# Optimization experiments

Measured on AMD Instinct MI355X. Metric: run time of the kernel, lower is better.

## Reference

```python
import jax, jax.numpy as jnp
import numpy as np

N = 50000          # nodes
E = 1_600_000      # edges
IN_DIM = 64
HID = 64
HEADS = 2
EDGE_DIM = 8
OUT_DIM = 2
NEG_SLOPE = 0.2    # PyG GATConv default negative_slope


def _gat_params(key, in_ch, out_ch, heads, edge_dim, concat):
    ks = jax.random.split(key, 6)
    s = 0.1
    W = jax.random.normal(ks[0], (in_ch, heads * out_ch), jnp.float32) * s
    a_src = jax.random.normal(ks[1], (heads, out_ch), jnp.float32) * s
    a_dst = jax.random.normal(ks[2], (heads, out_ch), jnp.float32) * s
    We = jax.random.normal(ks[3], (edge_dim, heads * out_ch), jnp.float32) * s
    a_e = jax.random.normal(ks[4], (heads, out_ch), jnp.float32) * s
    b = jnp.zeros((heads * out_ch if concat else out_ch,), jnp.float32)
    return W, a_src, a_dst, We, a_e, b


def gat_conv(x, edge_index, edge_attr, W, a_src, a_dst, We, a_e, b, heads, out_ch, concat):
    # Faithful PyG GATConv with edge_dim, add_self_loops=True, fill_value='mean'.
    n = x.shape[0]
    src0, dst0 = edge_index[0], edge_index[1]
    # self-loop edge_attr = mean of incoming edge attrs (scatter-mean over dst)
    cnt = jax.ops.segment_sum(jnp.ones((src0.shape[0],), x.dtype), dst0, num_segments=n)
    loop_attr = jax.ops.segment_sum(edge_attr, dst0, num_segments=n) / jnp.maximum(cnt, 1.0)[:, None]
    loop = jnp.arange(n, dtype=src0.dtype)
    src = jnp.concatenate([src0, loop])
    dst = jnp.concatenate([dst0, loop])
    ea = jnp.concatenate([edge_attr, loop_attr], axis=0)          # [E+N, edge_dim]

    h = (x @ W).reshape(n, heads, out_ch)                          # [N, H, C]
    al_src = jnp.einsum('nhc,hc->nh', h, a_src)                    # [N, H]
    al_dst = jnp.einsum('nhc,hc->nh', h, a_dst)
    e = (ea @ We).reshape(-1, heads, out_ch)                       # [E+N, H, C]
    al_edge = jnp.einsum('ehc,hc->eh', e, a_e)

    alpha = jax.nn.leaky_relu(al_src[src] + al_dst[dst] + al_edge, NEG_SLOPE)  # [E+N, H]
    # segment softmax over destination node (every dst has a self loop)
    amax = jax.ops.segment_max(alpha, dst, num_segments=n)
    ex = jnp.exp(alpha - amax[dst])
    denom = jax.ops.segment_sum(ex, dst, num_segments=n)
    w = ex / (denom[dst] + 1e-16)

    out = jax.ops.segment_sum(h[src] * w[:, :, None], dst, num_segments=n)     # [N, H, C]
    out = out.reshape(n, heads * out_ch) if concat else out.mean(axis=1)
    return out + b


def setup_inputs() -> dict:
    key = jax.random.key(0)
    ks = jax.random.split(key, 8)
    inp = {
        'x': jax.random.normal(ks[0], (N, IN_DIM), jnp.float32),
        'edge_index': jax.random.randint(ks[1], (2, E), 0, N, dtype=jnp.int32),
        'edge_attr': jax.random.normal(ks[2], (E, EDGE_DIM), jnp.float32),
    }
    # layer 0: in -> hid, heads=1, concat=True
    for name, p in zip(['W0', 'as0', 'ad0', 'We0', 'ae0', 'b0'], _gat_params(ks[3], IN_DIM, HID, 1, EDGE_DIM, True)):
        inp[name] = p
    # layers 1,2: hid -> hid, heads=HEADS, concat=False
    for name, p in zip(['W1', 'as1', 'ad1', 'We1', 'ae1', 'b1'], _gat_params(ks[4], HID, HID, HEADS, EDGE_DIM, False)):
        inp[name] = p
    for name, p in zip(['W2', 'as2', 'ad2', 'We2', 'ae2', 'b2'], _gat_params(ks[5], HID, HID, HEADS, EDGE_DIM, False)):
        inp[name] = p
    # final: hid -> out_dim, heads=1, concat=True
    for name, p in zip(['W3', 'as3', 'ad3', 'We3', 'ae3', 'b3'], _gat_params(ks[6], HID, OUT_DIM, 1, EDGE_DIM, True)):
        inp[name] = p
    return inp


def reference(x, edge_index, edge_attr,
              W0, as0, ad0, We0, ae0, b0,
              W1, as1, ad1, We1, ae1, b1,
              W2, as2, ad2, We2, ae2, b2,
              W3, as3, ad3, We3, ae3, b3):
    h = jax.nn.relu(gat_conv(x, edge_index, edge_attr, W0, as0, ad0, We0, ae0, b0, 1, HID, True))
    h = jax.nn.relu(gat_conv(h, edge_index, edge_attr, W1, as1, ad1, We1, ae1, b1, HEADS, HID, False))
    h = jax.nn.relu(gat_conv(h, edge_index, edge_attr, W2, as2, ad2, We2, ae2, b2, HEADS, HID, False))
    return gat_conv(h, edge_index, edge_attr, W3, as3, ad3, We3, ae3, b3, 1, OUT_DIM, True)
```

## Files before the change

### kernel.cpp

```cpp
#include <hip/hip_runtime.h>
#include <math.h>


#define GSZ 256
#define CAPB 10240
#define CHUNK 4096
#define CAP_C 9984

__device__ __forceinline__ float wave_sum64(float v) {
#pragma unroll
  for (int o = 32; o >= 1; o >>= 1) v += __shfl_xor(v, o);
  return v;
}
__device__ __forceinline__ float dot8(const float4& a, const float4& b,
                                      const float* c) {
  return a.x * c[0] + a.y * c[1] + a.z * c[2] + a.w * c[3] + b.x * c[4] +
         b.y * c[5] + b.z * c[6] + b.w * c[7];
}


__global__ __launch_bounds__(256) void bin_kernel(const int* __restrict__ src,
                                                  const int* __restrict__ dst,
                                                  int* __restrict__ bfill,
                                                  int2* __restrict__ bbuf,
                                                  int E_) {
  __shared__ int histo[256];
  __shared__ int scanb[256];
  __shared__ int segstart[256];
  __shared__ int gbase[256];
  __shared__ int cur[256];
  __shared__ int2 stage[CHUNK];
  __shared__ int gtarg[CHUNK];
  const int t = threadIdx.x;
  const int e0 = blockIdx.x * CHUNK;
  const int cnt = min(CHUNK, E_ - e0);
  histo[t] = 0;
  __syncthreads();
  int myd[CHUNK / 256];
#pragma unroll
  for (int k = 0; k < CHUNK / 256; ++k) {
    int i = t + k * 256;
    int d = -1;
    if (i < cnt) {
      d = dst[e0 + i];
      atomicAdd(&histo[d >> 8], 1);
    }
    myd[k] = d;
  }
  __syncthreads();
  const int v = histo[t];
  int acc = v;
  scanb[t] = v;
  __syncthreads();
#pragma unroll
  for (int o = 1; o < 256; o <<= 1) {
    int u = (t >= o) ? scanb[t - o] : 0;
    __syncthreads();
    acc += u;
    scanb[t] = acc;
    __syncthreads();
  }
  int gp = 0;
  if (v > 0) gp = atomicAdd(&bfill[t], v);
  segstart[t] = acc - v;
  gbase[t] = t * CAPB + min(gp, CAPB - v);
  cur[t] = 0;
  __syncthreads();
#pragma unroll
  for (int k = 0; k < CHUNK / 256; ++k) {
    int i = t + k * 256;
    int d = myd[k];
    if (d >= 0) {
      int b = d >> 8;
      int s = src[e0 + i];
      int p = atomicAdd(&cur[b], 1);
      int sl = segstart[b] + p;
      stage[sl] = make_int2(s, (e0 + i) | ((d & 255) << 21));
      gtarg[sl] = gbase[b] + p;
    }
  }
  __syncthreads();
  for (int i = t; i < cnt; i += 256) bbuf[gtarg[i]] = stage[i];
}

__global__ __launch_bounds__(256) void count_kernel(
    const int* __restrict__ bfill, const int2* __restrict__ bbuf,
    int* __restrict__ cnt, int n) {
  __shared__ int h[256];
  const int b = blockIdx.x;
  const int t = threadIdx.x;
  h[t] = 0;
  __syncthreads();
  const int m = min(bfill[b], CAPB);
  const int2* reg = bbuf + (size_t)b * CAPB;
  for (int i = t; i < m; i += 256) {
    int dl = ((unsigned)reg[i].y) >> 21;
    atomicAdd(&h[dl], 1);
  }
  __syncthreads();
  int node = b * GSZ + t;
  if (node < n) cnt[node] = h[t];
}

__global__ __launch_bounds__(256) void scan1_kernel(const int* __restrict__ cnt,
                                                    int* __restrict__ rowp,
                                                    int* __restrict__ bsum,
                                                    int n) {
  __shared__ int sd[256];
  const int t = threadIdx.x;
  const int base = blockIdx.x * 1024 + t * 4;
  int v0 = (base + 0 < n) ? cnt[base + 0] + 1 : 0;
  int v1 = (base + 1 < n) ? cnt[base + 1] + 1 : 0;
  int v2 = (base + 2 < n) ? cnt[base + 2] + 1 : 0;
  int v3 = (base + 3 < n) ? cnt[base + 3] + 1 : 0;
  const int s = v0 + v1 + v2 + v3;
  sd[t] = s;
  __syncthreads();
  int acc = s;
#pragma unroll
  for (int o = 1; o < 256; o <<= 1) {
    int u = (t >= o) ? sd[t - o] : 0;
    __syncthreads();
    acc += u;
    sd[t] = acc;
    __syncthreads();
  }
  int excl = acc - s;
  if (base + 0 < n) rowp[base + 0] = excl;
  if (base + 1 < n) rowp[base + 1] = excl + v0;
  if (base + 2 < n) rowp[base + 2] = excl + v0 + v1;
  if (base + 3 < n) rowp[base + 3] = excl + v0 + v1 + v2;
  if (t == 255) bsum[blockIdx.x] = acc;
}

__global__ void scan2_kernel(int* __restrict__ bsum, int nb) {
  const int lane = threadIdx.x;
  int v = (lane < nb) ? bsum[lane] : 0;
  int incl = v;
#pragma unroll
  for (int o = 1; o < 64; o <<= 1) {
    int u = __shfl_up(incl, o);
    if (lane >= o) incl += u;
  }
  if (lane < nb) bsum[lane] = incl - v;
  if (lane == 63) bsum[nb] = incl;
}

__global__ void scan3_kernel(int* __restrict__ rowp,
                             const int* __restrict__ bsum, int n, int nb) {
  int i = blockIdx.x * 256 + threadIdx.x;
  if (i >= n) return;
  rowp[i] += bsum[i >> 10];
  if (i == 0) rowp[n] = bsum[nb];
}

__global__ __launch_bounds__(256) void place_kernel(
    const int* __restrict__ rowp, const int* __restrict__ bfill,
    const int2* __restrict__ bbuf, int* __restrict__ col_src,
    int* __restrict__ eidA, int n, int E_) {
  __shared__ int rp[GSZ + 1];
  __shared__ int cur[GSZ];
  __shared__ int2 stage[CAP_C];
  const int b = blockIdx.x;
  const int t = threadIdx.x;
  const int lo = b * GSZ;
  const int nk = min(GSZ, n - lo);
  for (int i = t; i <= nk; i += 256) rp[i] = rowp[lo + i];
  cur[t] = 0;
  __syncthreads();
  const int s0 = rp[0];
  const int span = rp[nk] - s0;
  const bool fits = (span <= CAP_C);
  const int m = min(bfill[b], CAPB);
  const int2* reg = bbuf + (size_t)b * CAPB;
  for (int i = t; i < m; i += 256) {
    int2 pl = reg[i];
    int dl = ((unsigned)pl.y) >> 21;
    int e2 = pl.y & 0x1FFFFF;
    int p = atomicAdd(&cur[dl], 1);
    int slot = rp[dl] + p;
    if (fits) stage[slot - s0] = make_int2(pl.x, e2);
    else { col_src[slot] = pl.x; eidA[slot] = e2; }
  }
  if (t < nk) {
    int slot = rp[t + 1] - 1;
    int node = lo + t;
    if (fits) stage[slot - s0] = make_int2(node, E_ + node);
    else { col_src[slot] = node; eidA[slot] = E_ + node; }
  }
  __syncthreads();
  if (fits) {
    for (int i = t; i < span; i += 256) {
      int2 v = stage[i];
      col_src[s0 + i] = v.x;
      eidA[s0 + i] = v.y;
    }
  }
}

__global__ void comb_all_kernel(const float* __restrict__ We0,
                                const float* __restrict__ ae0,
                                const float* __restrict__ We1,
                                const float* __restrict__ ae1,
                                const float* __restrict__ We2,
                                const float* __restrict__ ae2,
                                const float* __restrict__ We3,
                                const float* __restrict__ ae3,
                                float* __restrict__ comb) {
  int t = threadIdx.x;
  if (t >= 48) return;
  float s = 0.f;
  if (t < 8) {
    int d = t;
    for (int c = 0; c < 64; ++c) s += We0[d * 64 + c] * ae0[c];
  } else if (t < 24) {
    int idx = t - 8, h = idx >> 3, d = idx & 7;
    for (int c = 0; c < 64; ++c) s += We1[d * 128 + h * 64 + c] * ae1[h * 64 + c];
  } else if (t < 40) {
    int idx = t - 24, h = idx >> 3, d = idx & 7;
    for (int c = 0; c < 64; ++c) s += We2[d * 128 + h * 64 + c] * ae2[h * 64 + c];
  } else {
    int d = t - 40;
    for (int c = 0; c < 2; ++c) s += We3[d * 2 + c] * ae3[c];
  }
  comb[t] = s;
}

__global__ __launch_bounds__(256) void edge_prep_kernel(
    const int* __restrict__ row_ptr, const int* __restrict__ eid,
    const float* __restrict__ ea, const float* __restrict__ comb,
    float* __restrict__ edot0, float* __restrict__ edot1,
    float* __restrict__ edot2, float* __restrict__ edot3, int n, int E_) {
  __shared__ float cb[48];
  if (threadIdx.x < 48) cb[threadIdx.x] = comb[threadIdx.x];
  __syncthreads();
  const int lane = threadIdx.x & 63;
  const int node = blockIdx.x * 4 + (threadIdx.x >> 6);
  if (node >= n) return;

  const int start = row_ptr[node];
  const int selfpos = row_ptr[node + 1] - 1;

  float s0 = 0.f, s1 = 0.f, s2 = 0.f, s3 = 0.f, s4 = 0.f, s5 = 0.f, s6 = 0.f,
        s7 = 0.f;
  for (int i = start + lane; i < selfpos; i += 64) {
    int id = eid[i];
    const float4* v = reinterpret_cast<const float4*>(ea + (size_t)id * 8);
    float4 a = v[0], b = v[1];
    s0 += a.x; s1 += a.y; s2 += a.z; s3 += a.w;
    s4 += b.x; s5 += b.y; s6 += b.z; s7 += b.w;
    edot0[i] = dot8(a, b, cb + 0);
    edot1[2 * i + 0] = dot8(a, b, cb + 8);
    edot1[2 * i + 1] = dot8(a, b, cb + 16);
    edot2[2 * i + 0] = dot8(a, b, cb + 24);
    edot2[2 * i + 1] = dot8(a, b, cb + 32);
    edot3[i] = dot8(a, b, cb + 40);
  }
#pragma unroll
  for (int o = 32; o >= 1; o >>= 1) {
    s0 += __shfl_xor(s0, o); s1 += __shfl_xor(s1, o);
    s2 += __shfl_xor(s2, o); s3 += __shfl_xor(s3, o);
    s4 += __shfl_xor(s4, o); s5 += __shfl_xor(s5, o);
    s6 += __shfl_xor(s6, o); s7 += __shfl_xor(s7, o);
  }
  if (lane == 0) {
    float deg = (float)(selfpos - start);
    float inv = 1.f / fmaxf(deg, 1.f);
    float4 a = make_float4(s0 * inv, s1 * inv, s2 * inv, s3 * inv);
    float4 b = make_float4(s4 * inv, s5 * inv, s6 * inv, s7 * inv);
    int i = selfpos;
    edot0[i] = dot8(a, b, cb + 0);
    edot1[2 * i + 0] = dot8(a, b, cb + 8);
    edot1[2 * i + 1] = dot8(a, b, cb + 16);
    edot2[2 * i + 0] = dot8(a, b, cb + 24);
    edot2[2 * i + 1] = dot8(a, b, cb + 32);
    edot3[i] = dot8(a, b, cb + 40);
  }
}


template <int HC, int H>
__global__ __launch_bounds__(256) void gemm_proj_kernel(
    const float* __restrict__ x, const float* __restrict__ W,
    const float* __restrict__ a_src, const float* __restrict__ a_dst,
    float* __restrict__ h, float* __restrict__ al_src,
    float* __restrict__ al_dst, int n) {
  constexpr int IN = 64;
  constexpr int C = HC / H;
  __shared__ float xs[32][IN];
  const int tid = threadIdx.x;
  const int j = tid % HC;
  const int rsub = tid / HC;
  constexpr int RPP = 256 / HC > 0 ? 256 / HC : 1;

  float wr[IN];
#pragma unroll
  for (int k = 0; k < IN; ++k) wr[k] = W[k * HC + j];
  const float asj = a_src[j];
  const float adj = a_dst[j];
  const int widx = (H == 2) ? (((j & (C - 1)) << 1) | (j >> 6)) : j;

  const int row0 = blockIdx.x * 32;
  {
    const float4* xv = reinterpret_cast<const float4*>(x);
    float4* xsv = reinterpret_cast<float4*>(&xs[0][0]);
    for (int i = tid; i < 32 * IN / 4; i += 256) {
      int r = i / (IN / 4);
      int row = row0 + r;
      float4 v = make_float4(0.f, 0.f, 0.f, 0.f);
      if (row < n) v = xv[(size_t)row * (IN / 4) + (i % (IN / 4))];
      xsv[i] = v;
    }
  }
  __syncthreads();

  for (int rb = 0; rb < 32; rb += RPP) {
    int r = rb + rsub;
    if (r >= 32) break;
    int row = row0 + r;
    float acc = 0.f;
#pragma unroll
    for (int k4 = 0; k4 < IN / 4; ++k4) {
      float4 xv = *reinterpret_cast<const float4*>(&xs[r][k4 * 4]);
      acc += xv.x * wr[k4 * 4 + 0] + xv.y * wr[k4 * 4 + 1] +
             xv.z * wr[k4 * 4 + 2] + xv.w * wr[k4 * 4 + 3];
    }
    if (row < n) h[(size_t)row * HC + widx] = acc;
    float ps = acc * asj;
    float pd = acc * adj;
#pragma unroll
    for (int o = C / 2; o >= 1; o >>= 1) {
      ps += __shfl_xor(ps, o);
      pd += __shfl_xor(pd, o);
    }
    if (row < n && (j % C) == 0) {
      int hh = j / C;
      al_src[(size_t)row * H + hh] = ps;
      al_dst[(size_t)row * H + hh] = pd;
    }
  }
}

template <int H, int C, bool CONCAT, bool RELU>
__global__ __launch_bounds__(256) void gat_node_kernel(
    const int* __restrict__ row_ptr, const int* __restrict__ col_src,
    const float* __restrict__ edot, const float* __restrict__ h_proj,
    const float* __restrict__ al_src, const float* __restrict__ al_dst,
    const float* __restrict__ bias, float* __restrict__ out, int n) {
  const int lane = threadIdx.x & 63;
  const int node = blockIdx.x * 4 + (threadIdx.x >> 6);
  if (node >= n) return;

  float adn[H];
#pragma unroll
  for (int h = 0; h < H; ++h) adn[h] = al_dst[node * H + h];

  const int start = row_ptr[node];
  const int end = row_ptr[node + 1];

  float denp[H];
#pragma unroll
  for (int h = 0; h < H; ++h) denp[h] = 0.f;
  float4 acc4 = make_float4(0.f, 0.f, 0.f, 0.f);
  float accp = 0.f;

  const int sub = lane & 15;
  const int grp16 = lane >> 4;
  const int idx = lane & 31;
  const int grp32 = lane >> 5;

  for (int base = start; base < end; base += 64) {
    const int i = base + lane;
    const bool valid = (i < end);
    int s = 0;
    float ex[H];
    if (valid) {
      s = col_src[i];
      if (H == 1) {
        float a = al_src[s] + adn[0] + edot[i];
        a = (a > 0.f) ? a : 0.2f * a;
        ex[0] = __expf(a);
      } else {
        float2 as2 = *reinterpret_cast<const float2*>(al_src + s * 2);
        float2 ed = *reinterpret_cast<const float2*>(edot + (size_t)i * 2);
        float a0 = as2.x + adn[0] + ed.x;
        float a1 = as2.y + adn[1] + ed.y;
        a0 = (a0 > 0.f) ? a0 : 0.2f * a0;
        a1 = (a1 > 0.f) ? a1 : 0.2f * a1;
        ex[0] = __expf(a0);
        ex[1] = __expf(a1);
      }
    } else {
#pragma unroll
      for (int h = 0; h < H; ++h) ex[h] = 0.f;
    }
#pragma unroll
    for (int h = 0; h < H; ++h) denp[h] += ex[h];

    const int cntc = min(64, end - base);
    if (C == 2) {
      const int half = lane >> 1;
      const int ch = lane & 1;
#pragma unroll
      for (int sb = 0; sb < 2; ++sb) {
        int tt = sb * 32 + half;
        int sv = __shfl(s, tt);
        float w = __shfl(ex[0], tt);
        if (tt < cntc) accp += w * h_proj[sv * 2 + ch];
      }
    } else if (H == 1) {
      const int nit = (cntc + 3) >> 2;
      for (int it0 = 0; it0 < nit; it0 += 4) {
        float4 v[4];
        float w[4];
#pragma unroll
        for (int u = 0; u < 4; ++u) {
          int tt = (it0 + u) * 4 + grp16;
          int sv = __shfl(s, tt);
          w[u] = __shfl(ex[0], tt);
          v[u] = *reinterpret_cast<const float4*>(h_proj + (size_t)sv * 64 +
                                                  sub * 4);
        }
#pragma unroll
        for (int u = 0; u < 4; ++u) {
          acc4.x += w[u] * v[u].x; acc4.y += w[u] * v[u].y;
          acc4.z += w[u] * v[u].z; acc4.w += w[u] * v[u].w;
        }
      }
    } else {
      const int nit = (cntc + 1) >> 1;
      for (int it0 = 0; it0 < nit; it0 += 4) {
        float4 v[4];
        float w0[4], w1[4];
#pragma unroll
        for (int u = 0; u < 4; ++u) {
          int tt = (it0 + u) * 2 + grp32;
          int sv = __shfl(s, tt);
          w0[u] = __shfl(ex[0], tt);
          w1[u] = __shfl(ex[1], tt);
          v[u] = *reinterpret_cast<const float4*>(h_proj + (size_t)sv * 128 +
                                                  idx * 4);
        }
#pragma unroll
        for (int u = 0; u < 4; ++u) {
          acc4.x += w0[u] * v[u].x; acc4.y += w1[u] * v[u].y;
          acc4.z += w0[u] * v[u].z; acc4.w += w1[u] * v[u].w;
        }
      }
    }
  }

  float den[H];
#pragma unroll
  for (int h = 0; h < H; ++h) den[h] = wave_sum64(denp[h]);

  if (C == 2) {
#pragma unroll
    for (int o = 2; o <= 32; o <<= 1) accp += __shfl_xor(accp, o);
    if (lane < 2) {
      float v = accp / (den[0] + 1e-16f) + bias[lane];
      if (RELU) v = fmaxf(v, 0.f);
      out[node * 2 + lane] = v;
    }
  } else if (H == 1) {
    acc4.x += __shfl_xor(acc4.x, 16); acc4.x += __shfl_xor(acc4.x, 32);
    acc4.y += __shfl_xor(acc4.y, 16); acc4.y += __shfl_xor(acc4.y, 32);
    acc4.z += __shfl_xor(acc4.z, 16); acc4.z += __shfl_xor(acc4.z, 32);
    acc4.w += __shfl_xor(acc4.w, 16); acc4.w += __shfl_xor(acc4.w, 32);
    if (lane < 16) {
      float inv = 1.f / (den[0] + 1e-16f);
      float4 bv = *reinterpret_cast<const float4*>(bias + sub * 4);
      float4 o;
      o.x = acc4.x * inv + bv.x; o.y = acc4.y * inv + bv.y;
      o.z = acc4.z * inv + bv.z; o.w = acc4.w * inv + bv.w;
      if (RELU) {
        o.x = fmaxf(o.x, 0.f); o.y = fmaxf(o.y, 0.f);
        o.z = fmaxf(o.z, 0.f); o.w = fmaxf(o.w, 0.f);
      }
      *reinterpret_cast<float4*>(out + (size_t)node * 64 + sub * 4) = o;
    }
  } else {
    acc4.x += __shfl_xor(acc4.x, 32); acc4.y += __shfl_xor(acc4.y, 32);
    acc4.z += __shfl_xor(acc4.z, 32); acc4.w += __shfl_xor(acc4.w, 32);
    if (lane < 32) {
      float i0 = 1.f / (den[0] + 1e-16f);
      float i1 = 1.f / (den[1] + 1e-16f);
      float2 bv = *reinterpret_cast<const float2*>(bias + idx * 2);
      float o0 = (acc4.x * i0 + acc4.y * i1) * 0.5f + bv.x;
      float o1 = (acc4.z * i0 + acc4.w * i1) * 0.5f + bv.y;
      if (RELU) { o0 = fmaxf(o0, 0.f); o1 = fmaxf(o1, 0.f); }
      float2 o = make_float2(o0, o1);
      *reinterpret_cast<float2*>(out + (size_t)node * 64 + idx * 2) = o;
    }
  }
}


static inline size_t align_up(size_t v, size_t a) { return (v + a - 1) & ~(a - 1); }

extern "C" void kernel_launch(void* const* d_in, const int* in_sizes, int n_in,
                              void* d_out, int out_size, void* d_ws,
                              size_t ws_size, hipStream_t stream) {
  const float* x = (const float*)d_in[0];
  const int* ei = (const int*)d_in[1];
  const float* ea = (const float*)d_in[2];

  const int N = in_sizes[0] / 64;
  const int E = in_sizes[1] / 2;
  const int* src0 = ei;
  const int* dst0 = ei + E;
  const int M = E + N;

  const float* W[4] = {(const float*)d_in[3], (const float*)d_in[9],
                       (const float*)d_in[15], (const float*)d_in[21]};
  const float* As[4] = {(const float*)d_in[4], (const float*)d_in[10],
                        (const float*)d_in[16], (const float*)d_in[22]};
  const float* Ad[4] = {(const float*)d_in[5], (const float*)d_in[11],
                        (const float*)d_in[17], (const float*)d_in[23]};
  const float* We[4] = {(const float*)d_in[6], (const float*)d_in[12],
                        (const float*)d_in[18], (const float*)d_in[24]};
  const float* Ae[4] = {(const float*)d_in[7], (const float*)d_in[13],
                        (const float*)d_in[19], (const float*)d_in[25]};
  const float* B[4] = {(const float*)d_in[8], (const float*)d_in[14],
                       (const float*)d_in[20], (const float*)d_in[26]};

  char* p = (char*)d_ws;
  size_t off = 0;
  auto carve = [&](size_t bytes) {
    void* r = p + off;
    off = align_up(off + bytes, 256);
    return r;
  };
  const int NBK = (N + GSZ - 1) / GSZ;
  int* cnt = (int*)carve((size_t)N * 4);
  int* row_ptr = (int*)carve((size_t)(N + 1) * 4);
  int* bsum = (int*)carve((size_t)256 * 4);
  int* bfill = (int*)carve((size_t)NBK * 4);
  int2* bbuf = (int2*)carve((size_t)NBK * CAPB * 8);
  int* col_src = (int*)carve((size_t)M * 4);
  int* eid = (int*)carve((size_t)M * 4);
  float* comb = (float*)carve(256);
  float* edot0 = (float*)carve((size_t)M * 4);
  float* edot1 = (float*)carve((size_t)M * 8);
  float* edot2 = (float*)carve((size_t)M * 8);
  float* edot3 = (float*)carve((size_t)M * 4);
  float* al_src = (float*)carve((size_t)N * 2 * 4);
  float* al_dst = (float*)carve((size_t)N * 2 * 4);
  float* h_proj = (float*)carve((size_t)N * 128 * 4);
  float* buf_a = (float*)carve((size_t)N * 64 * 4);
  float* buf_b = (float*)carve((size_t)N * 64 * 4);
  (void)ws_size;

  const int nb = (N + 1023) / 1024;

  hipMemsetAsync(bfill, 0, (size_t)NBK * 4, stream);
  bin_kernel<<<(E + CHUNK - 1) / CHUNK, 256, 0, stream>>>(src0, dst0, bfill,
                                                          bbuf, E);
  count_kernel<<<NBK, 256, 0, stream>>>(bfill, bbuf, cnt, N);
  scan1_kernel<<<nb, 256, 0, stream>>>(cnt, row_ptr, bsum, N);
  scan2_kernel<<<1, 64, 0, stream>>>(bsum, nb);
  scan3_kernel<<<(N + 255) / 256, 256, 0, stream>>>(row_ptr, bsum, N, nb);
  place_kernel<<<NBK, 256, 0, stream>>>(row_ptr, bfill, bbuf, col_src, eid, N,
                                        E);
  comb_all_kernel<<<1, 64, 0, stream>>>(We[0], Ae[0], We[1], Ae[1], We[2],
                                        Ae[2], We[3], Ae[3], comb);
  edge_prep_kernel<<<(N + 3) / 4, 256, 0, stream>>>(
      row_ptr, eid, ea, comb, edot0, edot1, edot2, edot3, N, E);

  const int gemm_grid = (N + 31) / 32;
  const int node_grid = (N + 3) / 4;

  gemm_proj_kernel<64, 1><<<gemm_grid, 256, 0, stream>>>(
      x, W[0], As[0], Ad[0], h_proj, al_src, al_dst, N);
  gat_node_kernel<1, 64, true, true><<<node_grid, 256, 0, stream>>>(
      row_ptr, col_src, edot0, h_proj, al_src, al_dst, B[0], buf_a, N);

  gemm_proj_kernel<128, 2><<<gemm_grid, 256, 0, stream>>>(
      buf_a, W[1], As[1], Ad[1], h_proj, al_src, al_dst, N);
  gat_node_kernel<2, 64, false, true><<<node_grid, 256, 0, stream>>>(
      row_ptr, col_src, edot1, h_proj, al_src, al_dst, B[1], buf_b, N);

  gemm_proj_kernel<128, 2><<<gemm_grid, 256, 0, stream>>>(
      buf_b, W[2], As[2], Ad[2], h_proj, al_src, al_dst, N);
  gat_node_kernel<2, 64, false, true><<<node_grid, 256, 0, stream>>>(
      row_ptr, col_src, edot2, h_proj, al_src, al_dst, B[2], buf_a, N);

  gemm_proj_kernel<2, 1><<<gemm_grid, 256, 0, stream>>>(
      buf_a, W[3], As[3], Ad[3], h_proj, al_src, al_dst, N);
  gat_node_kernel<1, 2, true, false><<<node_grid, 256, 0, stream>>>(
      row_ptr, col_src, edot3, h_proj, al_src, al_dst, B[3], (float*)d_out, N);
}
```

Measured before the change: 487.2 us.

## Split two-head layers into per-head planar passes for cache-friendlier gathers

The GEMM now writes the two-head projection as two separate N×64 planes instead of an interleaved N×128 layout. Each two-head GAT layer runs as two per-head aggregation kernels: the first writes a normalized partial to a scratch buffer reusing the bin buffer, and the second combines it with bias and ReLU. The aim is to halve the random-gather working set per pass so it fits better in cache. The cost is reading the CSR, the scores and the edge terms twice, plus an extra partial write and read per layer.

```diff
diff --git a/kernel.cpp b/kernel.cpp
--- a/kernel.cpp
+++ b/kernel.cpp
@@ -298,7 +298,6 @@
   for (int k = 0; k < IN; ++k) wr[k] = W[k * HC + j];
   const float asj = a_src[j];
   const float adj = a_dst[j];
-  const int widx = (H == 2) ? (((j & (C - 1)) << 1) | (j >> 6)) : j;
 
   const int row0 = blockIdx.x * 32;
   {
@@ -325,7 +324,13 @@
       acc += xv.x * wr[k4 * 4 + 0] + xv.y * wr[k4 * 4 + 1] +
              xv.z * wr[k4 * 4 + 2] + xv.w * wr[k4 * 4 + 3];
     }
-    if (row < n) h[(size_t)row * HC + widx] = acc;
+    if (row < n) {
+      size_t oidx = (H == 2)
+                        ? ((size_t)(j >> 6) * ((size_t)n * 64) +
+                           (size_t)row * 64 + (j & 63))
+                        : ((size_t)row * HC + j);
+      h[oidx] = acc;
+    }
     float ps = acc * asj;
     float pd = acc * adj;
 #pragma unroll
@@ -341,7 +346,7 @@
   }
 }
 
-template <int H, int C, bool CONCAT, bool RELU>
+template <int C, bool RELU>
 __global__ __launch_bounds__(256) void gat_node_kernel(
     const int* __restrict__ row_ptr, const int* __restrict__ col_src,
     const float* __restrict__ edot, const float* __restrict__ h_proj,
@@ -351,51 +356,29 @@
   const int node = blockIdx.x * 4 + (threadIdx.x >> 6);
   if (node >= n) return;
 
-  float adn[H];
-#pragma unroll
-  for (int h = 0; h < H; ++h) adn[h] = al_dst[node * H + h];
-
+  const float adn = al_dst[node];
   const int start = row_ptr[node];
   const int end = row_ptr[node + 1];
 
-  float denp[H];
-#pragma unroll
-  for (int h = 0; h < H; ++h) denp[h] = 0.f;
+  float denp = 0.f;
   float4 acc4 = make_float4(0.f, 0.f, 0.f, 0.f);
   float accp = 0.f;
 
   const int sub = lane & 15;
   const int grp16 = lane >> 4;
-  const int idx = lane & 31;
-  const int grp32 = lane >> 5;
 
   for (int base = start; base < end; base += 64) {
     const int i = base + lane;
     const bool valid = (i < end);
     int s = 0;
-    float ex[H];
+    float ex = 0.f;
     if (valid) {
       s = col_src[i];
-      if (H == 1) {
-        float a = al_src[s] + adn[0] + edot[i];
-        a = (a > 0.f) ? a : 0.2f * a;
-        ex[0] = __expf(a);
-      } else {
-        float2 as2 = *reinterpret_cast<const float2*>(al_src + s * 2);
-        float2 ed = *reinterpret_cast<const float2*>(edot + (size_t)i * 2);
-        float a0 = as2.x + adn[0] + ed.x;
-        float a1 = as2.y + adn[1] + ed.y;
-        a0 = (a0 > 0.f) ? a0 : 0.2f * a0;
-        a1 = (a1 > 0.f) ? a1 : 0.2f * a1;
-        ex[0] = __expf(a0);
-        ex[1] = __expf(a1);
-      }
-    } else {
-#pragma unroll
-      for (int h = 0; h < H; ++h) ex[h] = 0.f;
-    }
-#pragma unroll
-    for (int h = 0; h < H; ++h) denp[h] += ex[h];
+      float a = al_src[s] + adn + edot[i];
+      a = (a > 0.f) ? a : 0.2f * a;
+      ex = __expf(a);
+    }
+    denp += ex;
 
     const int cntc = min(64, end - base);
     if (C == 2) {
@@ -405,10 +388,10 @@
       for (int sb = 0; sb < 2; ++sb) {
         int tt = sb * 32 + half;
         int sv = __shfl(s, tt);
-        float w = __shfl(ex[0], tt);
+        float w = __shfl(ex, tt);
         if (tt < cntc) accp += w * h_proj[sv * 2 + ch];
       }
-    } else if (H == 1) {
+    } else {
       const int nit = (cntc + 3) >> 2;
       for (int it0 = 0; it0 < nit; it0 += 4) {
         float4 v[4];
@@ -417,7 +400,7 @@
         for (int u = 0; u < 4; ++u) {
           int tt = (it0 + u) * 4 + grp16;
           int sv = __shfl(s, tt);
-          w[u] = __shfl(ex[0], tt);
+          w[u] = __shfl(ex, tt);
           v[u] = *reinterpret_cast<const float4*>(h_proj + (size_t)sv * 64 +
                                                   sub * 4);
         }
@@ -427,48 +410,26 @@
           acc4.z += w[u] * v[u].z; acc4.w += w[u] * v[u].w;
         }
       }
-    } else {
-      const int nit = (cntc + 1) >> 1;
-      for (int it0 = 0; it0 < nit; it0 += 4) {
-        float4 v[4];
-        float w0[4], w1[4];
-#pragma unroll
-        for (int u = 0; u < 4; ++u) {
-          int tt = (it0 + u) * 2 + grp32;
-          int sv = __shfl(s, tt);
-          w0[u] = __shfl(ex[0], tt);
-          w1[u] = __shfl(ex[1], tt);
-          v[u] = *reinterpret_cast<const float4*>(h_proj + (size_t)sv * 128 +
-                                                  idx * 4);
-        }
-#pragma unroll
-        for (int u = 0; u < 4; ++u) {
-          acc4.x += w0[u] * v[u].x; acc4.y += w1[u] * v[u].y;
-          acc4.z += w0[u] * v[u].z; acc4.w += w1[u] * v[u].w;
-        }
-      }
-    }
-  }
-
-  float den[H];
-#pragma unroll
-  for (int h = 0; h < H; ++h) den[h] = wave_sum64(denp[h]);
+    }
+  }
+
+  const float den = wave_sum64(denp);
 
   if (C == 2) {
 #pragma unroll
     for (int o = 2; o <= 32; o <<= 1) accp += __shfl_xor(accp, o);
     if (lane < 2) {
-      float v = accp / (den[0] + 1e-16f) + bias[lane];
+      float v = accp / (den + 1e-16f) + bias[lane];
       if (RELU) v = fmaxf(v, 0.f);
       out[node * 2 + lane] = v;
     }
-  } else if (H == 1) {
+  } else {
     acc4.x += __shfl_xor(acc4.x, 16); acc4.x += __shfl_xor(acc4.x, 32);
     acc4.y += __shfl_xor(acc4.y, 16); acc4.y += __shfl_xor(acc4.y, 32);
     acc4.z += __shfl_xor(acc4.z, 16); acc4.z += __shfl_xor(acc4.z, 32);
     acc4.w += __shfl_xor(acc4.w, 16); acc4.w += __shfl_xor(acc4.w, 32);
     if (lane < 16) {
-      float inv = 1.f / (den[0] + 1e-16f);
+      float inv = 1.f / (den + 1e-16f);
       float4 bv = *reinterpret_cast<const float4*>(bias + sub * 4);
       float4 o;
       o.x = acc4.x * inv + bv.x; o.y = acc4.y * inv + bv.y;
@@ -479,18 +440,87 @@
       }
       *reinterpret_cast<float4*>(out + (size_t)node * 64 + sub * 4) = o;
     }
-  } else {
-    acc4.x += __shfl_xor(acc4.x, 32); acc4.y += __shfl_xor(acc4.y, 32);
-    acc4.z += __shfl_xor(acc4.z, 32); acc4.w += __shfl_xor(acc4.w, 32);
-    if (lane < 32) {
-      float i0 = 1.f / (den[0] + 1e-16f);
-      float i1 = 1.f / (den[1] + 1e-16f);
-      float2 bv = *reinterpret_cast<const float2*>(bias + idx * 2);
-      float o0 = (acc4.x * i0 + acc4.y * i1) * 0.5f + bv.x;
-      float o1 = (acc4.z * i0 + acc4.w * i1) * 0.5f + bv.y;
-      if (RELU) { o0 = fmaxf(o0, 0.f); o1 = fmaxf(o1, 0.f); }
-      float2 o = make_float2(o0, o1);
-      *reinterpret_cast<float2*>(out + (size_t)node * 64 + idx * 2) = o;
+  }
+}
+
+template <bool FIRST>
+__global__ __launch_bounds__(256) void gat_head_kernel(
+    const int* __restrict__ row_ptr, const int* __restrict__ col_src,
+    const float* __restrict__ edot2, int head,
+    const float* __restrict__ hplane, const float* __restrict__ al_src2,
+    const float* __restrict__ al_dst2, const float* __restrict__ bias,
+    float* __restrict__ partial, float* __restrict__ out, int n) {
+  const int lane = threadIdx.x & 63;
+  const int node = blockIdx.x * 4 + (threadIdx.x >> 6);
+  if (node >= n) return;
+
+  const float adn = al_dst2[node * 2 + head];
+  const int start = row_ptr[node];
+  const int end = row_ptr[node + 1];
+
+  float denp = 0.f;
+  float4 acc4 = make_float4(0.f, 0.f, 0.f, 0.f);
+
+  const int sub = lane & 15;
+  const int grp16 = lane >> 4;
+
+  for (int base = start; base < end; base += 64) {
+    const int i = base + lane;
+    const bool valid = (i < end);
+    int s = 0;
+    float ex = 0.f;
+    if (valid) {
+      s = col_src[i];
+      float a = al_src2[s * 2 + head] + adn + edot2[(size_t)i * 2 + head];
+      a = (a > 0.f) ? a : 0.2f * a;
+      ex = __expf(a);
+    }
+    denp += ex;
+
+    const int cntc = min(64, end - base);
+    const int nit = (cntc + 3) >> 2;
+    for (int it0 = 0; it0 < nit; it0 += 4) {
+      float4 v[4];
+      float w[4];
+#pragma unroll
+      for (int u = 0; u < 4; ++u) {
+        int tt = (it0 + u) * 4 + grp16;
+        int sv = __shfl(s, tt);
+        w[u] = __shfl(ex, tt);
+        v[u] = *reinterpret_cast<const float4*>(hplane + (size_t)sv * 64 +
+                                                sub * 4);
+      }
+#pragma unroll
+      for (int u = 0; u < 4; ++u) {
+        acc4.x += w[u] * v[u].x; acc4.y += w[u] * v[u].y;
+        acc4.z += w[u] * v[u].z; acc4.w += w[u] * v[u].w;
+      }
+    }
+  }
+
+  const float den = wave_sum64(denp);
+
+  acc4.x += __shfl_xor(acc4.x, 16); acc4.x += __shfl_xor(acc4.x, 32);
+  acc4.y += __shfl_xor(acc4.y, 16); acc4.y += __shfl_xor(acc4.y, 32);
+  acc4.z += __shfl_xor(acc4.z, 16); acc4.z += __shfl_xor(acc4.z, 32);
+  acc4.w += __shfl_xor(acc4.w, 16); acc4.w += __shfl_xor(acc4.w, 32);
+  if (lane < 16) {
+    float inv = 1.f / (den + 1e-16f);
+    if (FIRST) {
+      float4 o;
+      o.x = acc4.x * inv; o.y = acc4.y * inv;
+      o.z = acc4.z * inv; o.w = acc4.w * inv;
+      *reinterpret_cast<float4*>(partial + (size_t)node * 64 + sub * 4) = o;
+    } else {
+      float4 p =
+          *reinterpret_cast<const float4*>(partial + (size_t)node * 64 + sub * 4);
+      float4 bv = *reinterpret_cast<const float4*>(bias + sub * 4);
+      float4 o;
+      o.x = fmaxf((p.x + acc4.x * inv) * 0.5f + bv.x, 0.f);
+      o.y = fmaxf((p.y + acc4.y * inv) * 0.5f + bv.y, 0.f);
+      o.z = fmaxf((p.z + acc4.z * inv) * 0.5f + bv.z, 0.f);
+      o.w = fmaxf((p.w + acc4.w * inv) * 0.5f + bv.w, 0.f);
+      *reinterpret_cast<float4*>(out + (size_t)node * 64 + sub * 4) = o;
     }
   }
 }
@@ -549,6 +579,7 @@
   float* h_proj = (float*)carve((size_t)N * 128 * 4);
   float* buf_a = (float*)carve((size_t)N * 64 * 4);
   float* buf_b = (float*)carve((size_t)N * 64 * 4);
+  float* partial = (float*)bbuf;
   (void)ws_size;
 
   const int nb = (N + 1023) / 1024;
@@ -569,24 +600,33 @@
 
   const int gemm_grid = (N + 31) / 32;
   const int node_grid = (N + 3) / 4;
+  const size_t plane = (size_t)N * 64;
 
   gemm_proj_kernel<64, 1><<<gemm_grid, 256, 0, stream>>>(
       x, W[0], As[0], Ad[0], h_proj, al_src, al_dst, N);
-  gat_node_kernel<1, 64, true, true><<<node_grid, 256, 0, stream>>>(
+  gat_node_kernel<64, true><<<node_grid, 256, 0, stream>>>(
       row_ptr, col_src, edot0, h_proj, al_src, al_dst, B[0], buf_a, N);
 
   gemm_proj_kernel<128, 2><<<gemm_grid, 256, 0, stream>>>(
       buf_a, W[1], As[1], Ad[1], h_proj, al_src, al_dst, N);
-  gat_node_kernel<2, 64, false, true><<<node_grid, 256, 0, stream>>>(
-      row_ptr, col_src, edot1, h_proj, al_src, al_dst, B[1], buf_b, N);
+  gat_head_kernel<true><<<node_grid, 256, 0, stream>>>(
+      row_ptr, col_src, edot1, 0, h_proj, al_src, al_dst, B[1], partial,
+      nullptr, N);
+  gat_head_kernel<false><<<node_grid, 256, 0, stream>>>(
+      row_ptr, col_src, edot1, 1, h_proj + plane, al_src, al_dst, B[1],
+      partial, buf_b, N);
 
   gemm_proj_kernel<128, 2><<<gemm_grid, 256, 0, stream>>>(
       buf_b, W[2], As[2], Ad[2], h_proj, al_src, al_dst, N);
-  gat_node_kernel<2, 64, false, true><<<node_grid, 256, 0, stream>>>(
-      row_ptr, col_src, edot2, h_proj, al_src, al_dst, B[2], buf_a, N);
+  gat_head_kernel<true><<<node_grid, 256, 0, stream>>>(
+      row_ptr, col_src, edot2, 0, h_proj, al_src, al_dst, B[2], partial,
+      nullptr, N);
+  gat_head_kernel<false><<<node_grid, 256, 0, stream>>>(
+      row_ptr, col_src, edot2, 1, h_proj + plane, al_src, al_dst, B[2],
+      partial, buf_a, N);
 
   gemm_proj_kernel<2, 1><<<gemm_grid, 256, 0, stream>>>(
       buf_a, W[3], As[3], Ad[3], h_proj, al_src, al_dst, N);
-  gat_node_kernel<1, 2, true, false><<<node_grid, 256, 0, stream>>>(
+  gat_node_kernel<2, false><<<node_grid, 256, 0, stream>>>(
       row_ptr, col_src, edot3, h_proj, al_src, al_dst, B[3], (float*)d_out, N);
 }
```

Result: no change. 479.8 us (-1.5%).
